# Performance work log

Measured on AMD Instinct MI355X. Metric: run time of the kernel, lower is better.

The kernel has to match this reference:

```python
import jax, jax.numpy as jnp
import numpy as np

B, C4, N, L4 = 8, 64, 512, 12
CQ = C4 // 4  # conv output channels


def setup_inputs() -> dict:
    key = jax.random.key(0)
    k_x, k_wc, k_bc, k_wg, k_bg = jax.random.split(key, 5)
    x = jax.random.normal(k_x, (B, C4, N, L4), dtype=jnp.float32)
    # Conv2d(in_dim, in_dim//4, kernel_size=(1,1)) -> pointwise: weight (CQ, C4)
    W_conv = jax.random.normal(k_wc, (CQ, C4), dtype=jnp.float32) / np.sqrt(C4)
    b_conv = jax.random.normal(k_bc, (CQ,), dtype=jnp.float32) * 0.01
    # Linear(in_dim, in_dim)
    W_gcn = jax.random.normal(k_wg, (C4, C4), dtype=jnp.float32) / np.sqrt(C4)
    b_gcn = jax.random.normal(k_bg, (C4,), dtype=jnp.float32) * 0.01
    return {"x": x, "W_conv": W_conv, "b_conv": b_conv, "W_gcn": W_gcn, "b_gcn": b_gcn}


def reference(x, W_conv, b_conv, W_gcn, b_gcn):
    # --- SpatioTemporalCorrelationComputation ---
    # 1x1 conv over channels: (b,c4,n,l) -> (b,cq,n,l)
    Fc = jnp.einsum('oc,bcnl->bonl', W_conv, x) + b_conv[None, :, None, None]
    Fl = Fc[:, :, :, -1]                                   # b,cq,n (last time step)
    xy = jnp.einsum('bcn,bcmt->bnmt', Fl, Fc)              # b,n,n,l4
    xx = jnp.sqrt(jnp.einsum('bcn,bcn->bc', Fl, Fl))       # b,cq
    yy = jnp.sqrt(jnp.einsum('bcnt,bcnt->bc', Fc, Fc))     # b,cq
    l2 = jnp.einsum('bc,bc->b', xx, yy)[:, None, None, None]
    S = xy / l2                                            # b,n,n,l4

    # --- RelationalFeatureExtraction ---
    # Loop-based R[:, :, :, k] = sum_j S[:,k,None,:,j] * F4[:,:,:,j]
    # is exactly this single contraction (Se expansion never materialized):
    R = jnp.einsum('bknj,bcnj->bcnk', S, x)                # b,c4,n,n

    # --- GraphOperation ---
    A = jax.nn.relu(jnp.tanh(jnp.max(R, axis=1)))          # b,n,n
    xg = jnp.einsum('bcnk,bkn->bck', R, A)                 # b,c4,n
    # Linear over channel dim: Fg[b,o,k] = sum_c xg[b,c,k] W[o,c] + bias[o]
    Fg = jnp.einsum('bck,oc->bok', xg, W_gcn) + b_gcn[None, :, None]
    return Fg[..., None]                                   # b,c4,n,1
```

## Files before the change

kernel.cpp:

```cpp
#include <hip/hip_runtime.h>
#include <hip/hip_bf16.h>
#include <math.h>

#define B    8
#define C4   64
#define CQ   16
#define NN   512
#define L4   12
#define KT   128
#define XSP  100

#define O_TH   0
#define O_TL   (O_TH + (size_t)B*1024*NN/2)
#define O_T2H  (O_TL + (size_t)B*1024*NN/2)
#define O_T2L  (O_T2H + (size_t)B*NN*1024/2)
#define O_FL   (O_T2L + (size_t)B*NN*1024/2)
#define O_FLTH (O_FL + (size_t)B*CQ*NN)
#define O_FLTL (O_FLTH + (size_t)B*NN*16/2)
#define O_XX   (O_FLTL + (size_t)B*NN*16/2)
#define O_YY   (O_XX + B*CQ)
#define O_L2   (O_YY + B*CQ)
#define O_AH   (O_L2 + 16)
#define O_AL   (O_AH + (size_t)B*NN*NN/2)
#define O_XG   (O_AL + (size_t)B*NN*NN/2)
#define O_FCG  (O_XG + (size_t)B*C4*NN)

typedef __attribute__((ext_vector_type(8))) short short8;
typedef __attribute__((ext_vector_type(4))) float floatx4;
typedef __attribute__((ext_vector_type(16))) float floatx16;

__device__ inline void split2(float x0, float x1, uint& hw, uint& lw) {
  uint u0 = __float_as_uint(x0), u1 = __float_as_uint(x1);
  uint h0 = u0 >> 16, h1 = u1 >> 16;
  float r0 = x0 - __uint_as_float(h0 << 16);
  float r1 = x1 - __uint_as_float(h1 << 16);
  hw = h0 | (h1 << 16);
  lw = (__float_as_uint(r0) >> 16) | ((__float_as_uint(r1) >> 16) << 16);
}

__global__ __launch_bounds__(256) void k1a_fc(const float* __restrict__ x,
                                              const float* __restrict__ Wc,
                                              const float* __restrict__ bc,
                                              float* __restrict__ ws) {
  int id = blockIdx.x;
  int b = id & 7;
  int nch = id >> 3;
  int n0 = nch * 8;
  int t = threadIdx.x;
  __shared__ __align__(16) float xs[C4*XSP];
  __shared__ float wcs[CQ*65];
  __shared__ float bcs[CQ];
  __shared__ __align__(16) float fcs[8*CQ*L4];

  for (int e = t; e < CQ*C4; e += 256) {
    int q = e >> 6, c = e & 63;
    wcs[q*65 + c] = Wc[e];
  }
  if (t < CQ) bcs[t] = bc[t];
  const float* xb = x + (size_t)b*C4*NN*L4 + (size_t)n0*L4;
  for (int f = t; f < C4*24; f += 256) {
    int c = f / 24, r = f - c*24;
    float4 v = *(const float4*)(xb + (size_t)c*NN*L4 + r*4);
    *(float4*)(xs + c*XSP + r*4) = v;
  }
  __syncthreads();
  {
    int q = t & 15, slot = t >> 4;
    float accv[6];
    #pragma unroll
    for (int i = 0; i < 6; ++i) accv[i] = bcs[q];
    for (int c = 0; c < C4; ++c) {
      float wv = wcs[q*65 + c];
      const float* xc = xs + c*XSP;
      #pragma unroll
      for (int i = 0; i < 6; ++i) accv[i] += wv * xc[slot + 16*i];
    }
    #pragma unroll
    for (int i = 0; i < 6; ++i) {
      int nj = slot + 16*i;
      int nl = nj / L4, j = nj - nl*L4;
      fcs[nl*(CQ*L4) + q*L4 + j] = accv[i];
      if (j == L4-1) ws[O_FL + ((size_t)b*CQ + q)*NN + n0 + nl] = accv[i];
    }
  }
  __syncthreads();
  if (t < CQ) {
    float yy = 0.f, xx = 0.f;
    for (int nl = 0; nl < 8; ++nl) {
      #pragma unroll
      for (int j = 0; j < L4; ++j) { float v = fcs[nl*(CQ*L4) + t*L4 + j]; yy += v*v; }
      float w = fcs[nl*(CQ*L4) + t*L4 + (L4-1)];
      xx += w*w;
    }
    atomicAdd(ws + O_YY + b*CQ + t, yy);
    atomicAdd(ws + O_XX + b*CQ + t, xx);
  }
  float* fcg = ws + O_FCG + (size_t)(b*64 + nch)*1536;
  for (int f = t; f < 384; f += 256)
    *(float4*)(fcg + f*4) = *(const float4*)(fcs + f*4);
}

__global__ __launch_bounds__(256, 4) void k1t_T(const float* __restrict__ x,
                                                float* __restrict__ ws) {
  int id = blockIdx.x;
  int b = id & 7;
  int nch = id >> 3;
  int n0 = nch * 8;
  int t = threadIdx.x;
  __shared__ __align__(16) float xs[C4*XSP];
  __shared__ __align__(16) float fcs[8*CQ*L4];
  const float* xb = x + (size_t)b*C4*NN*L4 + (size_t)n0*L4;
  for (int f = t; f < C4*24; f += 256) {
    int c = f / 24, r = f - c*24;
    float4 v = *(const float4*)(xb + (size_t)c*NN*L4 + r*4);
    *(float4*)(xs + c*XSP + r*4) = v;
  }
  {
    const float* fcg = ws + O_FCG + (size_t)(b*64 + nch)*1536;
    for (int f = t; f < 384; f += 256)
      *(float4*)(fcs + f*4) = *(const float4*)(fcg + f*4);
  }
  __syncthreads();
  int c = t >> 2, q0 = (t & 3) * 4;
  float vals[4][8];
  ushort* T2H = (ushort*)(ws + O_T2H);
  ushort* T2L = (ushort*)(ws + O_T2L);
  for (int nl = 0; nl < 8; ++nl) {
    float xr[L4];
    *(float4*)&xr[0] = *(const float4*)(xs + c*XSP + nl*L4);
    *(float4*)&xr[4] = *(const float4*)(xs + c*XSP + nl*L4 + 4);
    *(float4*)&xr[8] = *(const float4*)(xs + c*XSP + nl*L4 + 8);
    float tvp[4];
    #pragma unroll
    for (int i = 0; i < 4; ++i) {
      const float* fq = fcs + nl*(CQ*L4) + (q0+i)*L4;
      float a = 0.f;
      #pragma unroll
      for (int j = 0; j < L4; ++j) a += fq[j] * xr[j];
      tvp[i] = a;
      vals[i][nl] = a;
    }
    uint hw0, lw0, hw1, lw1;
    split2(tvp[0], tvp[1], hw0, lw0);
    split2(tvp[2], tvp[3], hw1, lw1);
    size_t off2 = ((size_t)b*NN + n0 + nl)*1024 + t*4;
    *(uint2*)(T2H + off2) = make_uint2(hw0, hw1);
    *(uint2*)(T2L + off2) = make_uint2(lw0, lw1);
  }
  ushort* TH = (ushort*)(ws + O_TH);
  ushort* TL = (ushort*)(ws + O_TL);
  #pragma unroll
  for (int i = 0; i < 4; ++i) {
    int m = c*16 + q0 + i;
    uint hw[4], lw[4];
    #pragma unroll
    for (int jj = 0; jj < 4; ++jj)
      split2(vals[i][2*jj], vals[i][2*jj+1], hw[jj], lw[jj]);
    size_t off = ((size_t)b*1024 + m)*NN + n0;
    *(uint4*)(TH + off) = make_uint4(hw[0], hw[1], hw[2], hw[3]);
    *(uint4*)(TL + off) = make_uint4(lw[0], lw[1], lw[2], lw[3]);
  }
}

__global__ __launch_bounds__(256) void k1b_l2flt(float* __restrict__ ws) {
  int t = threadIdx.x;
  if (blockIdx.x == 0) {
    __shared__ float s[B*CQ];
    if (t < B*CQ) s[t] = sqrtf(ws[O_XX + t]) * sqrtf(ws[O_YY + t]);
    __syncthreads();
    if (t < B) {
      float sum = 0.f;
      #pragma unroll
      for (int q = 0; q < CQ; ++q) sum += s[t*CQ + q];
      ws[O_L2 + t] = 1.0f / sum;
    }
  }
  int idx = blockIdx.x*256 + t;
  int b = idx >> 9, k = idx & 511;
  const float* fl = ws + O_FL + (size_t)b*CQ*NN + k;
  ushort h[16], l[16];
  #pragma unroll
  for (int q = 0; q < CQ; ++q) {
    float v = fl[(size_t)q*NN];
    uint u = __float_as_uint(v);
    uint hh = u >> 16;
    float r = v - __uint_as_float(hh << 16);
    h[q] = (ushort)hh;
    l[q] = (ushort)(__float_as_uint(r) >> 16);
  }
  ushort* FH  = (ushort*)(ws + O_FLTH) + (size_t)idx*16;
  ushort* FLo = (ushort*)(ws + O_FLTL) + (size_t)idx*16;
  *(uint4*)(FH)      = *(uint4*)&h[0];
  *(uint4*)(FH + 8)  = *(uint4*)&h[8];
  *(uint4*)(FLo)     = *(uint4*)&l[0];
  *(uint4*)(FLo + 8) = *(uint4*)&l[8];
}

__global__ __launch_bounds__(256, 4) void k2_mfma(float* __restrict__ ws) {
  int id = blockIdx.x;
  int b = id & 7;
  int rest = id >> 3;
  int kh = rest & 1;
  int nch = rest >> 1;
  int t = threadIdx.x;
  int w = t >> 6, lane = t & 63;
  int col = lane & 31, half = lane >> 5;
  float l2inv = ws[O_L2 + b];
  const ushort* FltH = (const ushort*)(ws + O_FLTH);
  const ushort* FltL = (const ushort*)(ws + O_FLTL);
  short8 bhf[2], blf[2];
  int kcol[2];
  #pragma unroll
  for (int kt = 0; kt < 2; ++kt) {
    kcol[kt] = kh*256 + w*64 + kt*32 + col;
    size_t off = ((size_t)(b*NN + kcol[kt]))*16 + half*8;
    bhf[kt] = *(const short8*)(FltH + off);
    blf[kt] = *(const short8*)(FltL + off);
  }
  const ushort* T2H = (const ushort*)(ws + O_T2H) + ((size_t)b*NN + nch*8)*1024;
  const ushort* T2L = (const ushort*)(ws + O_T2L) + ((size_t)b*NN + nch*8)*1024;
  ushort* AH = (ushort*)(ws + O_AH) + ((size_t)b*NN + nch*8)*NN;
  ushort* AL = (ushort*)(ws + O_AL) + ((size_t)b*NN + nch*8)*NN;

  for (int i = 0; i < 8; ++i) {
    short8 ah[2], al[2];
    #pragma unroll
    for (int ct = 0; ct < 2; ++ct) {
      size_t off = (size_t)i*1024 + (ct*32 + col)*16 + half*8;
      ah[ct] = *(const short8*)(T2H + off);
      al[ct] = *(const short8*)(T2L + off);
    }
    floatx16 acc[2][2];
    #pragma unroll
    for (int ct = 0; ct < 2; ++ct)
      #pragma unroll
      for (int kt = 0; kt < 2; ++kt) {
        floatx16 a = {0.f,0.f,0.f,0.f,0.f,0.f,0.f,0.f,
                      0.f,0.f,0.f,0.f,0.f,0.f,0.f,0.f};
        a = __builtin_amdgcn_mfma_f32_32x32x16_bf16(ah[ct], bhf[kt], a, 0, 0, 0);
        a = __builtin_amdgcn_mfma_f32_32x32x16_bf16(ah[ct], blf[kt], a, 0, 0, 0);
        a = __builtin_amdgcn_mfma_f32_32x32x16_bf16(al[ct], bhf[kt], a, 0, 0, 0);
        acc[ct][kt] = a;
      }
    #pragma unroll
    for (int kt = 0; kt < 2; ++kt) {
      float m = acc[0][kt][0];
      #pragma unroll
      for (int ct = 0; ct < 2; ++ct)
        #pragma unroll
        for (int rg = 0; rg < 16; ++rg)
          if (ct + rg) m = fmaxf(m, acc[ct][kt][rg]);
      m = fmaxf(m, __shfl_xor(m, 32));
      float av = fmaxf(tanhf(m*l2inv), 0.f);
      uint u = __float_as_uint(av);
      uint hh = u >> 16;
      float r = av - __uint_as_float(hh << 16);
      ushort lv = (ushort)(__float_as_uint(r) >> 16);
      if (half == 0) {
        AH[(size_t)i*NN + kcol[kt]] = (ushort)hh;
        AL[(size_t)i*NN + kcol[kt]] = lv;
      }
    }
  }
}

__global__ __launch_bounds__(256, 2) void k3_mfma(float* __restrict__ ws) {
  int id = blockIdx.x;
  int b = id & 7;
  int rest = id >> 3;
  int kb = rest & 7;
  int mbb = rest >> 3;
  int t = threadIdx.x;
  int lane = t & 63;
  int w = t >> 6;
  int mw = w >> 1, kw = w & 1;
  int row = lane & 15, quad = lane >> 4;

  __shared__ __align__(16) ushort Ah[128*32];
  __shared__ __align__(16) ushort Al[128*32];
  __shared__ __align__(16) ushort Bh[64*32];
  __shared__ __align__(16) ushort Bl[64*32];

  const ushort* TH = (const ushort*)(ws + O_TH) + ((size_t)b*1024 + mbb*128)*NN;
  const ushort* TL = (const ushort*)(ws + O_TL) + ((size_t)b*1024 + mbb*128)*NN;
  const ushort* AHp = (const ushort*)(ws + O_AH) + ((size_t)b*NN + kb*64)*NN;
  const ushort* ALp = (const ushort*)(ws + O_AL) + ((size_t)b*NN + kb*64)*NN;

  floatx4 acc[4][2];
  #pragma unroll
  for (int i = 0; i < 4; ++i)
    #pragma unroll
    for (int j = 0; j < 2; ++j) acc[i][j] = (floatx4){0.f, 0.f, 0.f, 0.f};

  for (int ksx = 0; ksx < 16; ++ksx) {
    int p0 = ksx*32;
    __syncthreads();
    #pragma unroll
    for (int i = 0; i < 2; ++i) {
      int f = t + 256*i;
      int m = f >> 2, seg = (f & 3) * 8;
      *(uint4*)(Ah + m*32 + seg) = *(const uint4*)(TH + (size_t)m*NN + p0 + seg);
      *(uint4*)(Al + m*32 + seg) = *(const uint4*)(TL + (size_t)m*NN + p0 + seg);
    }
    {
      int j = t >> 2, seg = (t & 3) * 8;
      *(uint4*)(Bh + j*32 + seg) = *(const uint4*)(AHp + (size_t)j*NN + p0 + seg);
      *(uint4*)(Bl + j*32 + seg) = *(const uint4*)(ALp + (size_t)j*NN + p0 + seg);
    }
    __syncthreads();
    short8 bh[2], bl[2];
    #pragma unroll
    for (int kt = 0; kt < 2; ++kt) {
      int jrow = kw*32 + kt*16 + row;
      bh[kt] = *(const short8*)(Bh + jrow*32 + quad*8);
      bl[kt] = *(const short8*)(Bl + jrow*32 + quad*8);
    }
    #pragma unroll
    for (int mt = 0; mt < 4; ++mt) {
      int mrow = mw*64 + mt*16 + row;
      short8 ah = *(const short8*)(Ah + mrow*32 + quad*8);
      short8 al = *(const short8*)(Al + mrow*32 + quad*8);
      #pragma unroll
      for (int kt = 0; kt < 2; ++kt) {
        acc[mt][kt] = __builtin_amdgcn_mfma_f32_16x16x32_bf16(ah, bh[kt], acc[mt][kt], 0, 0, 0);
        acc[mt][kt] = __builtin_amdgcn_mfma_f32_16x16x32_bf16(ah, bl[kt], acc[mt][kt], 0, 0, 0);
        acc[mt][kt] = __builtin_amdgcn_mfma_f32_16x16x32_bf16(al, bh[kt], acc[mt][kt], 0, 0, 0);
      }
    }
  }
  float l2inv = ws[O_L2 + b];
  const float* flb = ws + O_FL + (size_t)b*CQ*NN;
  float fl[2][4];
  #pragma unroll
  for (int kt = 0; kt < 2; ++kt) {
    int kcol = kb*64 + kw*32 + kt*16 + row;
    #pragma unroll
    for (int rg = 0; rg < 4; ++rg)
      fl[kt][rg] = flb[(size_t)(quad*4 + rg)*NN + kcol];
  }
  #pragma unroll
  for (int mt = 0; mt < 4; ++mt) {
    int c = mbb*8 + mw*4 + mt;
    #pragma unroll
    for (int kt = 0; kt < 2; ++kt) {
      float s = fl[kt][0]*acc[mt][kt][0] + fl[kt][1]*acc[mt][kt][1]
              + fl[kt][2]*acc[mt][kt][2] + fl[kt][3]*acc[mt][kt][3];
      s += __shfl_xor(s, 32);
      s += __shfl_xor(s, 16);
      if (quad == 0) {
        int kcol = kb*64 + kw*32 + kt*16 + row;
        ws[O_XG + ((size_t)b*C4 + c)*NN + kcol] = s * l2inv;
      }
    }
  }
}

__global__ __launch_bounds__(256) void k4_out(const float* __restrict__ Wg,
                                              const float* __restrict__ bg,
                                              const float* __restrict__ ws,
                                              float* __restrict__ out) {
  int blk = blockIdx.x;
  int b = blk >> 2, kc = blk & 3;
  int t = threadIdx.x;
  __shared__ float xg[C4][KT+1];
  __shared__ float wg[C4*C4];
  for (int e = t; e < C4*C4; e += 256) wg[e] = Wg[e];
  for (int e = t; e < C4*KT; e += 256) {
    int c = e >> 7, kk = e & (KT-1);
    xg[c][kk] = ws[O_XG + ((size_t)(b*C4 + c))*NN + kc*KT + kk];
  }
  __syncthreads();
  int kk = t & (KT-1);
  int ohalf = t >> 7;
  for (int oi = 0; oi < 32; ++oi) {
    int o = ohalf*32 + oi;
    float acc = bg[o];
    #pragma unroll
    for (int c = 0; c < C4; ++c) acc += wg[o*C4 + c] * xg[c][kk];
    out[((size_t)(b*C4 + o))*NN + kc*KT + kk] = acc;
  }
}

extern "C" void kernel_launch(void* const* d_in, const int* in_sizes, int n_in,
                              void* d_out, int out_size, void* d_ws, size_t ws_size,
                              hipStream_t stream) {
  const float* x  = (const float*)d_in[0];
  const float* Wc = (const float*)d_in[1];
  const float* bc = (const float*)d_in[2];
  const float* Wg = (const float*)d_in[3];
  const float* bg = (const float*)d_in[4];
  float* ws  = (float*)d_ws;
  float* out = (float*)d_out;

  hipMemsetAsync(ws + O_XX, 0, (2*B*CQ + 16)*sizeof(float), stream);

  k1a_fc   <<<B*64,   256, 0, stream>>>(x, Wc, bc, ws);
  k1b_l2flt<<<16,     256, 0, stream>>>(ws);
  k1t_T    <<<B*64,   256, 0, stream>>>(x, ws);
  k2_mfma  <<<B*128,  256, 0, stream>>>(ws);
  k3_mfma  <<<B*64,   256, 0, stream>>>(ws);
  k4_out   <<<B*4,    256, 0, stream>>>(Wg, bg, ws, out);
}
```

Baseline: 152.8 us.

## Fuse T computation into Fc kernel and add separate LDS transpose kernel

```diff
diff --git a/kernel.cpp b/kernel.cpp
--- a/kernel.cpp
+++ b/kernel.cpp
@@ -23,7 +23,6 @@
 #define O_AH   (O_L2 + 16)
 #define O_AL   (O_AH + (size_t)B*NN*NN/2)
 #define O_XG   (O_AL + (size_t)B*NN*NN/2)
-#define O_FCG  (O_XG + (size_t)B*C4*NN)
 
 typedef __attribute__((ext_vector_type(8))) short short8;
 typedef __attribute__((ext_vector_type(4))) float floatx4;
@@ -38,10 +37,10 @@
   lw = (__float_as_uint(r0) >> 16) | ((__float_as_uint(r1) >> 16) << 16);
 }
 
-__global__ __launch_bounds__(256) void k1a_fc(const float* __restrict__ x,
-                                              const float* __restrict__ Wc,
-                                              const float* __restrict__ bc,
-                                              float* __restrict__ ws) {
+__global__ __launch_bounds__(256, 4) void k1_fc(const float* __restrict__ x,
+                                                const float* __restrict__ Wc,
+                                                const float* __restrict__ bc,
+                                                float* __restrict__ ws) {
   int id = blockIdx.x;
   int b = id & 7;
   int nch = id >> 3;
@@ -95,70 +94,64 @@
     atomicAdd(ws + O_YY + b*CQ + t, yy);
     atomicAdd(ws + O_XX + b*CQ + t, xx);
   }
-  float* fcg = ws + O_FCG + (size_t)(b*64 + nch)*1536;
-  for (int f = t; f < 384; f += 256)
-    *(float4*)(fcg + f*4) = *(const float4*)(fcs + f*4);
-}
-
-__global__ __launch_bounds__(256, 4) void k1t_T(const float* __restrict__ x,
-                                                float* __restrict__ ws) {
+  {
+    int c = t >> 2, q0 = (t & 3) * 4;
+    ushort* T2H = (ushort*)(ws + O_T2H);
+    ushort* T2L = (ushort*)(ws + O_T2L);
+    for (int nl = 0; nl < 8; ++nl) {
+      float xr[L4];
+      *(float4*)&xr[0] = *(const float4*)(xs + c*XSP + nl*L4);
+      *(float4*)&xr[4] = *(const float4*)(xs + c*XSP + nl*L4 + 4);
+      *(float4*)&xr[8] = *(const float4*)(xs + c*XSP + nl*L4 + 8);
+      float tvp[4];
+      #pragma unroll
+      for (int i = 0; i < 4; ++i) {
+        const float* fq = fcs + nl*(CQ*L4) + (q0+i)*L4;
+        float a = 0.f;
+        #pragma unroll
+        for (int j = 0; j < L4; ++j) a += fq[j] * xr[j];
+        tvp[i] = a;
+      }
+      uint hw0, lw0, hw1, lw1;
+      split2(tvp[0], tvp[1], hw0, lw0);
+      split2(tvp[2], tvp[3], hw1, lw1);
+      size_t off2 = ((size_t)b*NN + n0 + nl)*1024 + t*4;
+      *(uint2*)(T2H + off2) = make_uint2(hw0, hw1);
+      *(uint2*)(T2L + off2) = make_uint2(lw0, lw1);
+    }
+  }
+}
+
+__global__ __launch_bounds__(256) void k1tr(float* __restrict__ ws) {
   int id = blockIdx.x;
   int b = id & 7;
-  int nch = id >> 3;
-  int n0 = nch * 8;
-  int t = threadIdx.x;
-  __shared__ __align__(16) float xs[C4*XSP];
-  __shared__ __align__(16) float fcs[8*CQ*L4];
-  const float* xb = x + (size_t)b*C4*NN*L4 + (size_t)n0*L4;
-  for (int f = t; f < C4*24; f += 256) {
-    int c = f / 24, r = f - c*24;
-    float4 v = *(const float4*)(xb + (size_t)c*NN*L4 + r*4);
-    *(float4*)(xs + c*XSP + r*4) = v;
-  }
+  int rest = id >> 3;
+  int nt = rest & 15;
+  int mt = rest >> 4;
+  int t = threadIdx.x;
+  __shared__ ushort tile[2][32][33];
+  const ushort* T2H = (const ushort*)(ws + O_T2H) + ((size_t)b*NN)*1024;
+  const ushort* T2L = (const ushort*)(ws + O_T2L) + ((size_t)b*NN)*1024;
+  ushort* TH = (ushort*)(ws + O_TH) + ((size_t)b*1024)*NN;
+  ushort* TL = (ushort*)(ws + O_TL) + ((size_t)b*1024)*NN;
   {
-    const float* fcg = ws + O_FCG + (size_t)(b*64 + nch)*1536;
-    for (int f = t; f < 384; f += 256)
-      *(float4*)(fcs + f*4) = *(const float4*)(fcg + f*4);
+    int row = t >> 3, cg = t & 7;
+    size_t src = (size_t)(nt*32 + row)*1024 + mt*32 + cg*4;
+    *(uint2*)&tile[0][row][cg*4] = *(const uint2*)(T2H + src);
+    *(uint2*)&tile[1][row][cg*4] = *(const uint2*)(T2L + src);
   }
   __syncthreads();
-  int c = t >> 2, q0 = (t & 3) * 4;
-  float vals[4][8];
-  ushort* T2H = (ushort*)(ws + O_T2H);
-  ushort* T2L = (ushort*)(ws + O_T2L);
-  for (int nl = 0; nl < 8; ++nl) {
-    float xr[L4];
-    *(float4*)&xr[0] = *(const float4*)(xs + c*XSP + nl*L4);
-    *(float4*)&xr[4] = *(const float4*)(xs + c*XSP + nl*L4 + 4);
-    *(float4*)&xr[8] = *(const float4*)(xs + c*XSP + nl*L4 + 8);
-    float tvp[4];
+  {
+    int mrow = t >> 3, ng = t & 7;
+    ushort vh[4], vl[4];
     #pragma unroll
     for (int i = 0; i < 4; ++i) {
-      const float* fq = fcs + nl*(CQ*L4) + (q0+i)*L4;
-      float a = 0.f;
-      #pragma unroll
-      for (int j = 0; j < L4; ++j) a += fq[j] * xr[j];
-      tvp[i] = a;
-      vals[i][nl] = a;
-    }
-    uint hw0, lw0, hw1, lw1;
-    split2(tvp[0], tvp[1], hw0, lw0);
-    split2(tvp[2], tvp[3], hw1, lw1);
-    size_t off2 = ((size_t)b*NN + n0 + nl)*1024 + t*4;
-    *(uint2*)(T2H + off2) = make_uint2(hw0, hw1);
-    *(uint2*)(T2L + off2) = make_uint2(lw0, lw1);
-  }
-  ushort* TH = (ushort*)(ws + O_TH);
-  ushort* TL = (ushort*)(ws + O_TL);
-  #pragma unroll
-  for (int i = 0; i < 4; ++i) {
-    int m = c*16 + q0 + i;
-    uint hw[4], lw[4];
-    #pragma unroll
-    for (int jj = 0; jj < 4; ++jj)
-      split2(vals[i][2*jj], vals[i][2*jj+1], hw[jj], lw[jj]);
-    size_t off = ((size_t)b*1024 + m)*NN + n0;
-    *(uint4*)(TH + off) = make_uint4(hw[0], hw[1], hw[2], hw[3]);
-    *(uint4*)(TL + off) = make_uint4(lw[0], lw[1], lw[2], lw[3]);
+      vh[i] = tile[0][ng*4 + i][mrow];
+      vl[i] = tile[1][ng*4 + i][mrow];
+    }
+    size_t dst = (size_t)(mt*32 + mrow)*NN + nt*32 + ng*4;
+    *(uint2*)(TH + dst) = *(uint2*)vh;
+    *(uint2*)(TL + dst) = *(uint2*)vl;
   }
 }
 
@@ -394,10 +387,10 @@
 
   hipMemsetAsync(ws + O_XX, 0, (2*B*CQ + 16)*sizeof(float), stream);
 
-  k1a_fc   <<<B*64,   256, 0, stream>>>(x, Wc, bc, ws);
-  k1b_l2flt<<<16,     256, 0, stream>>>(ws);
-  k1t_T    <<<B*64,   256, 0, stream>>>(x, ws);
-  k2_mfma  <<<B*128,  256, 0, stream>>>(ws);
-  k3_mfma  <<<B*64,   256, 0, stream>>>(ws);
-  k4_out   <<<B*4,    256, 0, stream>>>(Wg, bg, ws, out);
-}
+  k1_fc    <<<B*64,     256, 0, stream>>>(x, Wc, bc, ws);
+  k1b_l2flt<<<16,       256, 0, stream>>>(ws);
+  k1tr     <<<B*16*32,  256, 0, stream>>>(ws);
+  k2_mfma  <<<B*128,    256, 0, stream>>>(ws);
+  k3_mfma  <<<B*64,     256, 0, stream>>>(ws);
+  k4_out   <<<B*4,      256, 0, stream>>>(Wg, bg, ws, out);
+}
```

Measured after the change: 219.7 us. 1.44x slower.
